# Optimization experiments

Hardware: AMD Instinct MI355X
Metric: run time of the kernel (lower is better)

Reference implementation:

```python
import jax, jax.numpy as jnp
import numpy as np


def setup_inputs() -> dict:
    key = jax.random.key(0)
    k1, k2, k3, k4, k5 = jax.random.split(key, 5)
    B, N, E, C_in, C_out, K = 64, 4096, 16, 64, 64, 3
    return {
        "x": jax.random.normal(k1, (B, N, C_in), dtype=jnp.float32),
        "adj_matrix": jax.random.normal(k2, (N, E), dtype=jnp.float32),
        "adj_embeddings": jax.random.normal(k3, (E, N), dtype=jnp.float32),
        "weights": jax.random.normal(k4, (K, C_in, C_out), dtype=jnp.float32) * 0.1,
        "bias": jax.random.normal(k5, (C_out,), dtype=jnp.float32) * 0.1,
    }


def reference(x, adj_matrix, adj_embeddings, weights, bias):
    # x: [B, N, C_in]; adj_matrix: [N, E]; adj_embeddings: [E, N]
    N = adj_matrix.shape[0]
    cheb_k = weights.shape[0]
    # adaptive adjacency: softmax(relu(adj @ emb), axis=1) -> [N, N]
    supports = jax.nn.softmax(jax.nn.relu(adj_matrix @ adj_embeddings), axis=1)
    # Chebyshev polynomial recursion: T0 = I, T1 = supports,
    # Tk = 2*supports @ T_{k-1} - T_{k-2}
    support_set = [jnp.eye(N, dtype=supports.dtype), supports]
    for _ in range(2, cheb_k):
        support_set.append(2.0 * supports @ support_set[-1] - support_set[-2])
    supports_k = jnp.stack(support_set, axis=0)  # [K, N, N]
    # aggregate: [K,N,M] x [B,M,C] -> [B,N,K,C]
    x_g = jnp.einsum("knm,bmc->bnkc", supports_k, x)
    # mix: [B,N,K,Cin] x [K,Cin,Cout] -> [B,N,Cout]
    return jnp.einsum("bnki,kio->bno", x_g, weights) + bias
```

## Files before the change

### kernel.cpp

```cpp
#include <hip/hip_runtime.h>


typedef __bf16 bf16;
typedef __bf16 bf16x8 __attribute__((ext_vector_type(8)));
typedef float f32x4 __attribute__((ext_vector_type(4)));

__device__ __forceinline__ void async_lds16(const void* g, void* l) {
  __builtin_amdgcn_global_load_lds((const __attribute__((address_space(1))) void*)g,
                                   (__attribute__((address_space(3))) void*)l, 16, 0, 0);
}

#define FENCE() asm volatile("" ::: "memory")
#define BAR()                          \
  do {                                 \
    FENCE();                           \
    __builtin_amdgcn_s_barrier();      \
    FENCE();                           \
  } while (0)
#define WAIT_VM(n) asm volatile("s_waitcnt vmcnt(" #n ")" ::: "memory")

__global__ __launch_bounds__(256) void build_wcat_k(const float* __restrict__ w, bf16* __restrict__ Wc) {
  int idx = blockIdx.x * 256 + threadIdx.x;
  if (idx >= 64 * 192) return;
  int o = idx / 192, kk = idx - o * 192;
  int k = kk >> 6, i = kk & 63;
  float v;
  if (k == 0)      v = w[i * 64 + o] - w[2 * 4096 + i * 64 + o];
  else if (k == 1) v = w[4096 + i * 64 + o];
  else             v = 2.f * w[2 * 4096 + i * 64 + o];
  Wc[idx] = (bf16)v;
}

__global__ __launch_bounds__(256) void supports_k(const float* __restrict__ adj,
                                                  const float* __restrict__ emb,
                                                  bf16* __restrict__ S) {
  __shared__ float sadj[8][16];
  __shared__ float sred[4];
  const int tid = threadIdx.x;
  const int n0 = blockIdx.x * 8;
  if (tid < 128) sadj[tid >> 4][tid & 15] = adj[n0 * 16 + tid];
  __syncthreads();
  for (int r = 0; r < 8; ++r) {
    float vals[16];
    float mx = 0.f;
    #pragma unroll
    for (int it = 0; it < 16; ++it) {
      const int j = it * 256 + tid;
      float v = 0.f;
      #pragma unroll
      for (int e = 0; e < 16; ++e) v = fmaf(sadj[r][e], emb[e * 4096 + j], v);
      v = fmaxf(v, 0.f);
      vals[it] = v;
      mx = fmaxf(mx, v);
    }
    #pragma unroll
    for (int off = 32; off > 0; off >>= 1) mx = fmaxf(mx, __shfl_xor(mx, off, 64));
    if ((tid & 63) == 0) sred[tid >> 6] = mx;
    __syncthreads();
    mx = fmaxf(fmaxf(sred[0], sred[1]), fmaxf(sred[2], sred[3]));
    float sum = 0.f;
    #pragma unroll
    for (int it = 0; it < 16; ++it) {
      float ev = __expf(vals[it] - mx);
      vals[it] = ev;
      sum += ev;
    }
    #pragma unroll
    for (int off = 32; off > 0; off >>= 1) sum += __shfl_xor(sum, off, 64);
    __syncthreads();
    if ((tid & 63) == 0) sred[tid >> 6] = sum;
    __syncthreads();
    const float inv = 1.f / (sred[0] + sred[1] + sred[2] + sred[3]);
    bf16* Srow = S + (n0 + r) * 4096;
    #pragma unroll
    for (int it = 0; it < 16; ++it) Srow[it * 256 + tid] = (bf16)(vals[it] * inv);
    __syncthreads();
  }
}

__global__ __launch_bounds__(256) void xpose_x_k(const float* __restrict__ x, bf16* __restrict__ Xt) {
  __shared__ float tile[64][65];
  const int tid = threadIdx.x;
  const int mt = blockIdx.x, b = blockIdx.y;
  const float* src = x + (b * 4096 + mt * 64) * 64;
  #pragma unroll
  for (int it = 0; it < 16; ++it) {
    const int idx = it * 256 + tid;
    tile[idx >> 6][idx & 63] = src[idx];
  }
  __syncthreads();
  #pragma unroll
  for (int it = 0; it < 16; ++it) {
    const int idx = it * 256 + tid;
    const int rr = idx >> 6, cc = idx & 63;
    Xt[(b * 64 + rr) * 4096 + mt * 64 + cc] = (bf16)tile[cc][rr];
  }
}

__global__ __launch_bounds__(256) void transpose_bf16_k(const bf16* __restrict__ in, bf16* __restrict__ outT) {
  __shared__ bf16 tile[64][65];
  const int tid = threadIdx.x;
  const int ti = blockIdx.x & 63, tj = blockIdx.x >> 6;
  #pragma unroll
  for (int it = 0; it < 16; ++it) {
    const int idx = it * 256 + tid;
    tile[idx >> 6][idx & 63] = in[(ti * 64 + (idx >> 6)) * 4096 + tj * 64 + (idx & 63)];
  }
  __syncthreads();
  #pragma unroll
  for (int it = 0; it < 16; ++it) {
    const int idx = it * 256 + tid;
    const int rr = idx >> 6, cc = idx & 63;
    outT[(tj * 64 + rr) * 4096 + ti * 64 + cc] = tile[cc][rr];
  }
}

__global__ __launch_bounds__(512, 2) void gemm256_k(const bf16* __restrict__ A,
                                                    const bf16* __restrict__ Bt,
                                                    bf16* __restrict__ C,
                                                    bf16* __restrict__ Ct) {
  __shared__ bf16 As[2][2][256][32];
  __shared__ bf16 Bs[2][2][256][32];

  const int tid = threadIdx.x;
  const int bid = blockIdx.x;
  const int wg = (bid & 7) * 32 + (bid >> 3);
  const int tm = wg >> 4, tn = wg & 15;
  const int rowBase = tm * 256, colBase = tn * 256;

  const int wv = tid >> 6, lane = tid & 63;
  const int wm = wv >> 2, wn = wv & 3;
  const int t16 = lane & 15, quad = lane >> 4;
  const int wv16 = wv * 16;
  const int q8 = (quad ^ ((t16 >> 1) & 3)) * 8;
  const int wm128 = wm * 128;
  const int wn64 = wn * 64;

  const int sr = tid >> 2;
  const int sc = ((tid & 3) ^ ((tid >> 3) & 3)) * 8;
  const bf16* gA = A + (size_t)(rowBase + sr) * 4096 + sc;
  const bf16* gB = Bt + (size_t)(colBase + sr) * 4096 + sc;

  f32x4 acc[8][4];
  #pragma unroll
  for (int i = 0; i < 8; ++i)
    #pragma unroll
    for (int j = 0; j < 4; ++j) acc[i][j] = (f32x4){0.f, 0.f, 0.f, 0.f};

  auto stA = [&](int buf, int s, int k0) {
    async_lds16(gA + k0 + s * 32, &As[buf][s][wv16][0]);
    async_lds16(gA + 524288 + k0 + s * 32, &As[buf][s][128 + wv16][0]);
  };
  auto stB = [&](int buf, int s, int k0) {
    async_lds16(gB + k0 + s * 32, &Bs[buf][s][wv16][0]);
    async_lds16(gB + 524288 + k0 + s * 32, &Bs[buf][s][128 + wv16][0]);
  };

  bf16x8 Ra[4], Rb[4], B0[4], B1[4];
  auto rdA = [&](bf16x8* R, int buf, int s, int g) {
    #pragma unroll
    for (int i = 0; i < 4; ++i)
      R[i] = *(const bf16x8*)&As[buf][s][wm128 + (g * 4 + i) * 16 + t16][q8];
  };
  auto rdB = [&](bf16x8* R, int buf, int s) {
    #pragma unroll
    for (int j = 0; j < 4; ++j)
      R[j] = *(const bf16x8*)&Bs[buf][s][wn64 + j * 16 + t16][q8];
  };
  auto mfma16 = [&](int g, const bf16x8* R, const bf16x8* Bv) {
    __builtin_amdgcn_s_setprio(1);
    #pragma unroll
    for (int i = 0; i < 4; ++i)
      #pragma unroll
      for (int j = 0; j < 4; ++j)
        acc[g * 4 + i][j] =
            __builtin_amdgcn_mfma_f32_16x16x32_bf16(R[i], Bv[j], acc[g * 4 + i][j], 0, 0, 0);
    __builtin_amdgcn_s_setprio(0);
  };

  stB(0, 0, 0); stA(0, 0, 0); stB(0, 1, 0); stA(0, 1, 0);
  stB(1, 0, 64); stA(1, 0, 64); stB(1, 1, 64);
  WAIT_VM(6);
  BAR();

  for (int it = 0; it < 31; ++it) {
    const int kb = it * 128;
    rdA(Ra, 0, 0, 0); rdB(B0, 0, 0); rdA(Rb, 0, 0, 1);
    stA(1, 1, kb + 64);
    mfma16(0, Ra, B0);
    BAR();
    rdA(Ra, 0, 1, 0); rdB(B1, 0, 1);
    stB(0, 0, kb + 128);
    mfma16(1, Rb, B0);
    BAR();
    rdA(Rb, 0, 1, 1);
    stA(0, 0, kb + 128);
    mfma16(0, Ra, B1);
    BAR();
    stB(0, 1, kb + 128);
    mfma16(1, Rb, B1);
    WAIT_VM(6);
    BAR();
    rdA(Ra, 1, 0, 0); rdB(B0, 1, 0); rdA(Rb, 1, 0, 1);
    stA(0, 1, kb + 128);
    mfma16(0, Ra, B0);
    BAR();
    rdA(Ra, 1, 1, 0); rdB(B1, 1, 1);
    stB(1, 0, kb + 192);
    mfma16(1, Rb, B0);
    BAR();
    rdA(Rb, 1, 1, 1);
    stA(1, 0, kb + 192);
    mfma16(0, Ra, B1);
    BAR();
    stB(1, 1, kb + 192);
    mfma16(1, Rb, B1);
    WAIT_VM(6);
    BAR();
  }

  rdA(Ra, 0, 0, 0); rdB(B0, 0, 0); rdA(Rb, 0, 0, 1);
  stA(1, 1, 4032);
  mfma16(0, Ra, B0);
  BAR();
  rdA(Ra, 0, 1, 0); rdB(B1, 0, 1);
  mfma16(1, Rb, B0);
  BAR();
  rdA(Rb, 0, 1, 1);
  mfma16(0, Ra, B1);
  BAR();
  mfma16(1, Rb, B1);
  WAIT_VM(0);
  BAR();
  rdA(Ra, 1, 0, 0); rdB(B0, 1, 0); rdA(Rb, 1, 0, 1);
  mfma16(0, Ra, B0);
  rdA(Ra, 1, 1, 0); rdB(B1, 1, 1);
  mfma16(1, Rb, B0);
  rdA(Rb, 1, 1, 1);
  mfma16(0, Ra, B1);
  mfma16(1, Rb, B1);

  #pragma unroll
  for (int i = 0; i < 8; ++i) {
    const int row0 = rowBase + wm128 + i * 16 + quad * 4;
    #pragma unroll
    for (int j = 0; j < 4; ++j) {
      const int col = colBase + wn64 + j * 16 + t16;
      #pragma unroll
      for (int rr = 0; rr < 4; ++rr)
        C[(size_t)(row0 + rr) * 4096 + col] = (bf16)acc[i][j][rr];
    }
  }
  if (Ct) {
    #pragma unroll
    for (int i = 0; i < 8; ++i) {
      const int row0 = rowBase + wm128 + i * 16 + quad * 4;
      #pragma unroll
      for (int j = 0; j < 4; ++j) {
        const int col = colBase + wn64 + j * 16 + t16;
        union { bf16 h[4]; uint2 u; } pk;
        #pragma unroll
        for (int rr = 0; rr < 4; ++rr) pk.h[rr] = (bf16)acc[i][j][rr];
        *(uint2*)(Ct + (size_t)col * 4096 + row0) = pk.u;
      }
    }
  }
}

__global__ __launch_bounds__(256) void mix_k(const float* __restrict__ x, const bf16* __restrict__ XG1,
                                             const bf16* __restrict__ XG2, const bf16* __restrict__ Wc,
                                             const float* __restrict__ bias, float* __restrict__ out) {
  __shared__ bf16 sW[64 * 200];
  const int tid = threadIdx.x;
  const int nt = blockIdx.x, b = blockIdx.y;
  {
    const int rw = tid >> 2, part = tid & 3;
    #pragma unroll
    for (int v = 0; v < 6; ++v)
      *(bf16x8*)(sW + rw * 200 + part * 48 + v * 8) = *(const bf16x8*)(Wc + rw * 192 + part * 48 + v * 8);
  }
  __syncthreads();

  const int lane = tid & 63, wv = tid >> 6;
  const int t16 = lane & 15, quad = lane >> 4;
  const int nBase = nt * 128 + wv * 32;

  f32x4 acc[2][4];
  #pragma unroll
  for (int i = 0; i < 2; ++i)
    #pragma unroll
    for (int j = 0; j < 4; ++j) acc[i][j] = (f32x4){0.f, 0.f, 0.f, 0.f};

  #pragma unroll
  for (int ch = 0; ch < 6; ++ch) {
    bf16x8 a[2];
    #pragma unroll
    for (int i = 0; i < 2; ++i) {
      const int row = nBase + i * 16 + t16;
      if (ch < 2) {
        const float* p = x + (b * 4096 + row) * 64 + ch * 32 + quad * 8;
        float4 f0 = *(const float4*)p;
        float4 f1 = *(const float4*)(p + 4);
        bf16x8 t;
        t[0] = (bf16)f0.x; t[1] = (bf16)f0.y; t[2] = (bf16)f0.z; t[3] = (bf16)f0.w;
        t[4] = (bf16)f1.x; t[5] = (bf16)f1.y; t[6] = (bf16)f1.z; t[7] = (bf16)f1.w;
        a[i] = t;
      } else {
        const bf16* src = (ch < 4) ? XG1 : XG2;
        a[i] = *(const bf16x8*)(src + row * 4096 + b * 64 + (ch & 1) * 32 + quad * 8);
      }
    }
    #pragma unroll
    for (int j = 0; j < 4; ++j) {
      bf16x8 wf = *(const bf16x8*)(sW + (j * 16 + t16) * 200 + ch * 32 + quad * 8);
      #pragma unroll
      for (int i = 0; i < 2; ++i)
        acc[i][j] = __builtin_amdgcn_mfma_f32_16x16x32_bf16(a[i], wf, acc[i][j], 0, 0, 0);
    }
  }

  #pragma unroll
  for (int j = 0; j < 4; ++j) {
    const float bb = bias[j * 16 + t16];
    #pragma unroll
    for (int i = 0; i < 2; ++i) {
      const int n0 = nBase + i * 16 + quad * 4;
      #pragma unroll
      for (int rr = 0; rr < 4; ++rr)
        out[(b * 4096 + n0 + rr) * 64 + j * 16 + t16] = acc[i][j][rr] + bb;
    }
  }
}

extern "C" void kernel_launch(void* const* d_in, const int* in_sizes, int n_in,
                              void* d_out, int out_size, void* d_ws, size_t ws_size,
                              hipStream_t stream) {
  const float* x    = (const float*)d_in[0];
  const float* adj  = (const float*)d_in[1];
  const float* emb  = (const float*)d_in[2];
  const float* w    = (const float*)d_in[3];
  const float* bias = (const float*)d_in[4];
  float* out = (float*)d_out;

  char* ws = (char*)d_ws;
  const size_t SZ = (size_t)4096 * 4096 * sizeof(bf16);
  bf16* S    = (bf16*)(ws);
  bf16* XG1  = (bf16*)(ws + SZ);
  bf16* XG2  = (bf16*)(ws + 2 * SZ);
  bf16* XBUF = (bf16*)(ws + 3 * SZ);
  const bool fused_t = ws_size >= 5 * SZ + (size_t)(64 * 192 * sizeof(bf16));
  bf16* XG1T = fused_t ? (bf16*)(ws + 4 * SZ) : XBUF;
  bf16* Wc   = (bf16*)(ws + (fused_t ? 5 : 4) * SZ);

  build_wcat_k<<<48, 256, 0, stream>>>(w, Wc);
  supports_k<<<512, 256, 0, stream>>>(adj, emb, S);
  xpose_x_k<<<dim3(64, 64), 256, 0, stream>>>(x, XBUF);
  gemm256_k<<<256, 512, 0, stream>>>(S, XBUF, XG1, fused_t ? XG1T : nullptr);
  if (!fused_t) transpose_bf16_k<<<4096, 256, 0, stream>>>(XG1, XBUF);
  gemm256_k<<<256, 512, 0, stream>>>(S, XG1T, XG2, nullptr);
  mix_k<<<dim3(32, 64), 256, 0, stream>>>(x, XG1, XG2, Wc, bias, out);
}
```

Before: 434.1 us.

## Software-pipeline LDS fragment reads one phase ahead of MFMA in GEMM loop

Restructures the main bf16 MFMA loop so the LDS reads for the next phase's A/B fragments are issued before the current MFMA block, with explicit lgkmcnt waits before each barrier and the vmcnt waits moved earlier. This is meant to hide LDS read latency behind MFMA work and cut stalls at barriers. It risks more register pressure and extra waits. Correctness also depends on the reordered vmcnt thresholds still guaranteeing that buffers are filled before they are read.

```diff
diff --git a/kernel.cpp b/kernel.cpp
--- a/kernel.cpp
+++ b/kernel.cpp
@@ -18,6 +18,7 @@
     FENCE();                           \
   } while (0)
 #define WAIT_VM(n) asm volatile("s_waitcnt vmcnt(" #n ")" ::: "memory")
+#define LGKM0() asm volatile("s_waitcnt lgkmcnt(0)" ::: "memory")
 
 __global__ __launch_bounds__(256) void build_wcat_k(const float* __restrict__ w, bf16* __restrict__ Wc) {
   int idx = blockIdx.x * 256 + threadIdx.x;
@@ -182,57 +183,60 @@
   stB(1, 0, 64); stA(1, 0, 64); stB(1, 1, 64);
   WAIT_VM(6);
   BAR();
+  rdA(Ra, 0, 0, 0); rdB(B0, 0, 0);
 
   for (int it = 0; it < 31; ++it) {
     const int kb = it * 128;
-    rdA(Ra, 0, 0, 0); rdB(B0, 0, 0); rdA(Rb, 0, 0, 1);
+    rdA(Rb, 0, 0, 1);
     stA(1, 1, kb + 64);
     mfma16(0, Ra, B0);
-    BAR();
+    LGKM0(); BAR();
     rdA(Ra, 0, 1, 0); rdB(B1, 0, 1);
     stB(0, 0, kb + 128);
     mfma16(1, Rb, B0);
-    BAR();
+    LGKM0(); BAR();
     rdA(Rb, 0, 1, 1);
     stA(0, 0, kb + 128);
+    WAIT_VM(4);
     mfma16(0, Ra, B1);
-    BAR();
+    LGKM0(); BAR();
+    rdA(Ra, 1, 0, 0); rdB(B0, 1, 0);
     stB(0, 1, kb + 128);
     mfma16(1, Rb, B1);
-    WAIT_VM(6);
-    BAR();
-    rdA(Ra, 1, 0, 0); rdB(B0, 1, 0); rdA(Rb, 1, 0, 1);
+    LGKM0(); BAR();
+    rdA(Rb, 1, 0, 1);
     stA(0, 1, kb + 128);
     mfma16(0, Ra, B0);
-    BAR();
+    LGKM0(); BAR();
     rdA(Ra, 1, 1, 0); rdB(B1, 1, 1);
     stB(1, 0, kb + 192);
     mfma16(1, Rb, B0);
-    BAR();
+    LGKM0(); BAR();
     rdA(Rb, 1, 1, 1);
     stA(1, 0, kb + 192);
+    WAIT_VM(4);
     mfma16(0, Ra, B1);
-    BAR();
+    LGKM0(); BAR();
+    rdA(Ra, 0, 0, 0); rdB(B0, 0, 0);
     stB(1, 1, kb + 192);
     mfma16(1, Rb, B1);
-    WAIT_VM(6);
-    BAR();
-  }
-
-  rdA(Ra, 0, 0, 0); rdB(B0, 0, 0); rdA(Rb, 0, 0, 1);
+    LGKM0(); BAR();
+  }
+
+  rdA(Rb, 0, 0, 1);
   stA(1, 1, 4032);
   mfma16(0, Ra, B0);
-  BAR();
+  LGKM0(); BAR();
   rdA(Ra, 0, 1, 0); rdB(B1, 0, 1);
   mfma16(1, Rb, B0);
-  BAR();
+  LGKM0(); BAR();
   rdA(Rb, 0, 1, 1);
+  WAIT_VM(0);
   mfma16(0, Ra, B1);
-  BAR();
+  LGKM0(); BAR();
+  rdA(Ra, 1, 0, 0); rdB(B0, 1, 0);
   mfma16(1, Rb, B1);
-  WAIT_VM(0);
-  BAR();
-  rdA(Ra, 1, 0, 0); rdB(B0, 1, 0); rdA(Rb, 1, 0, 1);
+  rdA(Rb, 1, 0, 1);
   mfma16(0, Ra, B0);
   rdA(Ra, 1, 1, 0); rdB(B1, 1, 1);
   mfma16(1, Rb, B0);
```

Measured after the change: 459.6 us. +5.9%, slower.
